# Kernel optimization log

Hardware: AMD Instinct MI355X
Metric: run time of the kernel (lower is better)

## Reference

```python
import jax, jax.numpy as jnp
import numpy as np

# Static config (matches init_kwargs: dim=64, ffn=2.66, kernel=3, smk=3, heads=2)
DIM = 64
NUM_HEADS = 2
KS = 3
SMK = 3
POOL = 7           # ContMix pools context to 7x7 -> 49 context tokens
HIDDEN = 172       # round_up(int(64*2.66), 4)
HIDDEN2 = 2 * HIDDEN
CTX_DW = HIDDEN2 // 4   # 86
CTX_DW12 = HIDDEN // 4  # 43
NK = SMK * SMK + KS * KS  # 18


def conv1x1(x, w):
    # x: [B,C,H,W], w: [O,C] -> [B,O,H,W]
    return jnp.einsum('bchw,oc->bohw', x, w)


def extract_patches(x, k):
    # x: [B,C,H,W] -> [B,C,k*k,H,W], zero ('same') padding, stride 1
    p = k // 2
    B, C, H, W = x.shape
    xp = jnp.pad(x, ((0, 0), (0, 0), (p, p), (p, p)))
    pats = [xp[:, :, i:i + H, j:j + W] for i in range(k) for j in range(k)]
    return jnp.stack(pats, axis=2)


def dyn_dw(x, attn, k, heads):
    # Dynamic depthwise mixing: per-pixel, per-head k*k kernel shared across
    # channels within a head. x: [B,C,H,W], attn: [B,g,HW,k*k]
    B, C, H, W = x.shape
    hd = C // heads
    pat = extract_patches(x, k).reshape(B, heads, hd, k * k, H * W)
    out = jnp.einsum('bgdkn,bgnk->bgdn', pat, attn)
    return out.reshape(B, C, H, W)


def contmix(x, ctx, wq, wk, wp, wpb, wo):
    # Content-aware dynamic depthwise-mixing (ContMix, OverLoCK-style).
    B, C, H, W = x.shape
    hd_qk = (C // 2) // NUM_HEADS
    scale = hd_qk ** -0.5
    # query from x, key from 7x7-pooled context
    q = conv1x1(x, wq) * scale                     # [B, C//2, H, W]
    ph, pw = H // POOL, W // POOL
    ctx_p = ctx.reshape(B, -1, POOL, ph, POOL, pw).mean(axis=(3, 5))  # [B,ctx,7,7]
    key = conv1x1(ctx_p, wk)                       # [B, C//2, 7, 7]
    q = q.reshape(B, NUM_HEADS, hd_qk, H * W)
    key = key.reshape(B, NUM_HEADS, hd_qk, POOL * POOL)
    w = jnp.einsum('bgcn,bgcl->bgnl', q, key)      # [B,g,HW,49]
    # project 49 context scores -> smk^2 + k^2 dynamic kernel taps (1x1 conv w/ bias)
    w = jnp.einsum('bgnl,ol->bgno', w, wp) + wpb   # [B,g,HW,18]
    a1 = jax.nn.softmax(w[..., :SMK * SMK], axis=-1)
    a2 = jax.nn.softmax(w[..., SMK * SMK:], axis=-1)
    # first channel half mixed with small kernel, second half with large kernel
    x1, x2 = jnp.split(x, 2, axis=1)
    y = jnp.concatenate([dyn_dw(x1, a1, SMK, NUM_HEADS),
                         dyn_dw(x2, a2, KS, NUM_HEADS)], axis=1)
    return conv1x1(y, wo)


def setup_inputs() -> dict:
    key = jax.random.key(0)
    ks = jax.random.split(key, 32)
    def w(i, o, c):
        return jax.random.normal(ks[i], (o, c), dtype=jnp.float32) / np.sqrt(c)
    inp = {
        'x': jax.random.normal(ks[0], (2, DIM, 112, 112), dtype=jnp.float32),
        'pin_w': w(1, HIDDEN2, DIM),
        'ctx_w': w(2, CTX_DW, HIDDEN2),
        'ctx1_w': w(3, CTX_DW12, HIDDEN),
        'ctx2_w': w(4, CTX_DW12, HIDDEN),
        'pout_w': w(5, DIM, HIDDEN),
        # ContMix on hidden_x2 (dim=344, ctx=86)
        'cm0_q': w(6, HIDDEN2 // 2, HIDDEN2),
        'cm0_k': w(7, HIDDEN2 // 2, CTX_DW),
        'cm0_p': w(8, NK, POOL * POOL),
        'cm0_pb': jnp.zeros((NK,), dtype=jnp.float32),
        'cm0_o': w(9, HIDDEN2, HIDDEN2),
        # ContMix on hidden (dim=172, ctx=43) -- branch 1
        'cm1_q': w(10, HIDDEN // 2, HIDDEN),
        'cm1_k': w(11, HIDDEN // 2, CTX_DW12),
        'cm1_p': w(12, NK, POOL * POOL),
        'cm1_pb': jnp.zeros((NK,), dtype=jnp.float32),
        'cm1_o': w(13, HIDDEN, HIDDEN),
        # ContMix on hidden -- branch 2
        'cm2_q': w(14, HIDDEN // 2, HIDDEN),
        'cm2_k': w(15, HIDDEN // 2, CTX_DW12),
        'cm2_p': w(16, NK, POOL * POOL),
        'cm2_pb': jnp.zeros((NK,), dtype=jnp.float32),
        'cm2_o': w(17, HIDDEN, HIDDEN),
    }
    return inp


def reference(x, pin_w, ctx_w, ctx1_w, ctx2_w, pout_w,
              cm0_q, cm0_k, cm0_p, cm0_pb, cm0_o,
              cm1_q, cm1_k, cm1_p, cm1_pb, cm1_o,
              cm2_q, cm2_k, cm2_p, cm2_pb, cm2_o):
    x_in = conv1x1(x, pin_w)                           # [B, 2*hidden, H, W]
    ctx_dw = conv1x1(x_in, ctx_w)                      # [B, ctx_dw, H, W]
    x_dw = contmix(x_in, ctx_dw, cm0_q, cm0_k, cm0_p, cm0_pb, cm0_o)
    x1, x2 = jnp.split(x_dw, 2, axis=1)                # each [B, hidden, H, W]
    ctx1 = conv1x1(x1, ctx1_w)
    ctx2 = conv1x1(x2, ctx2_w)
    x1p = jnp.tanh(contmix(x1, ctx1, cm1_q, cm1_k, cm1_p, cm1_pb, cm1_o)) + x1
    x2p = jnp.tanh(contmix(x2, ctx2, cm2_q, cm2_k, cm2_p, cm2_pb, cm2_o)) + x2
    out = conv1x1(x1p * x2p, pout_w)                   # [B, dim, H, W]
    return out
```

## Files before the change

### kernel.cpp

```cpp
#include <hip/hip_runtime.h>
#include <math.h>

#define HW 12544
#define W_IMG 112
#define B_SZ 2

typedef __attribute__((ext_vector_type(8))) short s8v;
typedef __attribute__((ext_vector_type(4))) float f4v;

__device__ __forceinline__ void split_bf16(float x, unsigned short& h, unsigned short& l) {
    unsigned u  = __float_as_uint(x);
    unsigned hb = (u + 0x7FFFu + ((u >> 16) & 1u)) >> 16;
    float hf    = __uint_as_float(hb << 16);
    float r     = x - hf;
    unsigned ur = __float_as_uint(r);
    unsigned lb = (ur + 0x7FFFu + ((ur >> 16) & 1u)) >> 16;
    h = (unsigned short)hb; l = (unsigned short)lb;
}

struct WSplitArgs {
    const float* src[8];
    const float* src2[8];
    unsigned short* hi[8];
    unsigned short* lo[8];
    int O1[8]; int O2[8]; int O2B[8]; int K[8]; int Kp[8]; int MpKp[8];
    float scale2[8];
};

__global__ __launch_bounds__(256) void wsplit_k(WSplitArgs a) {
    const int ci  = blockIdx.y;
    const int idx = blockIdx.x * 256 + threadIdx.x;
    if (idx >= a.MpKp[ci]) return;
    const int Kp   = a.Kp[ci];
    const int blk  = 32 * Kp;
    const int mblk = idx / blk;
    const int rem  = idx - mblk * blk;
    const int kc   = rem >> 10;
    const int rem2 = rem & 1023;
    const int kq   = rem2 >> 8;
    const int row  = (rem2 >> 3) & 31;
    const int j    = rem2 & 7;
    const int o = mblk * 32 + row, k = kc * 32 + kq * 8 + j;
    float v = 0.f;
    if (k < a.K[ci]) {
        if (o < a.O1[ci])
            v = a.src[ci][(size_t)o * a.K[ci] + k];
        else if (o >= a.O2B[ci] && o - a.O2B[ci] < a.O2[ci])
            v = a.src2[ci][(size_t)(o - a.O2B[ci]) * a.K[ci] + k] * a.scale2[ci];
    }
    unsigned short h, l;
    split_bf16(v, h, l);
    a.hi[ci][idx] = h; a.lo[ci][idx] = l;
}

__global__ __launch_bounds__(256) void tsplit_k(
    const float* __restrict__ src, size_t bstride, int C, int KC,
    unsigned short* __restrict__ hi, unsigned short* __restrict__ lo)
{
    __shared__ __align__(16) float t[32][36];
    const int b   = blockIdx.z;
    const int hw0 = blockIdx.x * 32;
    const int kc  = blockIdx.y;
    const int c0  = kc * 32;
    const int tid = threadIdx.x;

    {
        const int cl = tid >> 3, hq = (tid & 7) * 4;
        const int c  = c0 + cl;
        float4 v = make_float4(0.f, 0.f, 0.f, 0.f);
        if (c < C)
            v = *(const float4*)(src + (size_t)b * bstride + (size_t)c * HW + hw0 + hq);
        *(float4*)&t[cl][hq] = v;
    }
    __syncthreads();

    const int hl = tid >> 3, cq = (tid & 7) * 4;
    float v0 = t[cq + 0][hl], v1 = t[cq + 1][hl], v2 = t[cq + 2][hl], v3 = t[cq + 3][hl];
    ushort4 h4, l4;
    split_bf16(v0, h4.x, l4.x);
    split_bf16(v1, h4.y, l4.y);
    split_bf16(v2, h4.z, l4.z);
    split_bf16(v3, h4.w, l4.w);
    const int ns = hw0 >> 8, r = (hw0 & 255) + hl;
    const int kq = cq >> 3, j0 = cq & 7;
    const size_t base = (((size_t)b * 49 + ns) * KC + kc) * 8192
                        + (size_t)kq * 2048 + (size_t)r * 8 + j0;
    *(ushort4*)(hi + base) = h4;
    *(ushort4*)(lo + base) = l4;
}

template <int KP>
__global__ __launch_bounds__(256) void gemm_k(
    const unsigned short* __restrict__ bt_hi, const unsigned short* __restrict__ bt_lo,
    const unsigned short* __restrict__ w_hi,  const unsigned short* __restrict__ w_lo,
    int per_m,
    float* __restrict__ outA, int OA, size_t oa_bstride,
    float* __restrict__ outB, int OB, size_t ob_bstride, int obase,
    int mode, int Ovalid,
    const float* __restrict__ res, size_t res_bstride,
    const float* __restrict__ mul, size_t mul_bstride)
{
    constexpr int KC = KP / 32;
    __shared__ __align__(16) unsigned short Bh_s[8192];
    __shared__ __align__(16) unsigned short Bl_s[8192];
    __shared__ __align__(16) unsigned short Ah_s[1024];
    __shared__ __align__(16) unsigned short Al_s[1024];

    const int b   = blockIdx.y;
    const int bx  = blockIdx.x;
    const int xcd = bx & 7, t = bx >> 3;
    const int m   = t % per_m;
    const int ns  = (t / per_m) * 8 + xcd;
    if (ns >= 49) return;

    const int tid  = threadIdx.x;
    const int wv   = tid >> 6, lane = tid & 63;
    const int m16  = lane & 15, quad = lane >> 4;
    const int mbase = m * 32;
    const int nbase = ns * 256 + wv * 64;

    const unsigned short* Bh_g = bt_hi + ((size_t)b * 49 + ns) * KC * 8192;
    const unsigned short* Bl_g = bt_lo + ((size_t)b * 49 + ns) * KC * 8192;
    const unsigned short* Ah_g = w_hi + (size_t)m * KC * 1024;
    const unsigned short* Al_g = w_lo + (size_t)m * KC * 1024;

    f4v acc[2][4];
#pragma unroll
    for (int mt = 0; mt < 2; ++mt)
#pragma unroll
        for (int f = 0; f < 4; ++f) acc[mt][f] = (f4v){0.f, 0.f, 0.f, 0.f};

    s8v rB[8], rA;
#pragma unroll
    for (int j = 0; j < 4; ++j) {
        rB[j]     = *(const s8v*)(Bh_g + (size_t)(j * 256 + tid) * 8);
        rB[4 + j] = *(const s8v*)(Bl_g + (size_t)(j * 256 + tid) * 8);
    }
    rA = (tid < 128) ? *(const s8v*)(Ah_g + (size_t)tid * 8)
                     : *(const s8v*)(Al_g + (size_t)(tid - 128) * 8);
#pragma unroll
    for (int j = 0; j < 4; ++j) {
        *(s8v*)(Bh_s + (j * 256 + tid) * 8) = rB[j];
        *(s8v*)(Bl_s + (j * 256 + tid) * 8) = rB[4 + j];
    }
    if (tid < 128) *(s8v*)(Ah_s + tid * 8) = rA;
    else           *(s8v*)(Al_s + (tid - 128) * 8) = rA;
    __syncthreads();

#pragma unroll
    for (int kc = 0; kc < KC; ++kc) {
        if (kc + 1 < KC) {
            const unsigned short* bh = Bh_g + (size_t)(kc + 1) * 8192;
            const unsigned short* bl = Bl_g + (size_t)(kc + 1) * 8192;
#pragma unroll
            for (int j = 0; j < 4; ++j) {
                rB[j]     = *(const s8v*)(bh + (size_t)(j * 256 + tid) * 8);
                rB[4 + j] = *(const s8v*)(bl + (size_t)(j * 256 + tid) * 8);
            }
            rA = (tid < 128)
                ? *(const s8v*)(Ah_g + (size_t)(kc + 1) * 1024 + (size_t)tid * 8)
                : *(const s8v*)(Al_g + (size_t)(kc + 1) * 1024 + (size_t)(tid - 128) * 8);
        }
#pragma unroll
        for (int mt = 0; mt < 2; ++mt) {
            s8v ah = *(const s8v*)(Ah_s + (quad * 32 + mt * 16 + m16) * 8);
            s8v al = *(const s8v*)(Al_s + (quad * 32 + mt * 16 + m16) * 8);
#pragma unroll
            for (int f = 0; f < 4; ++f) {
                const int row = wv * 64 + f * 16 + m16;
                s8v bh = *(const s8v*)(Bh_s + (quad * 256 + row) * 8);
                s8v bl = *(const s8v*)(Bl_s + (quad * 256 + row) * 8);
                acc[mt][f] = __builtin_amdgcn_mfma_f32_16x16x32_bf16(ah, bh, acc[mt][f], 0, 0, 0);
                acc[mt][f] = __builtin_amdgcn_mfma_f32_16x16x32_bf16(al, bh, acc[mt][f], 0, 0, 0);
                acc[mt][f] = __builtin_amdgcn_mfma_f32_16x16x32_bf16(ah, bl, acc[mt][f], 0, 0, 0);
            }
        }
        __syncthreads();
        if (kc + 1 < KC) {
#pragma unroll
            for (int j = 0; j < 4; ++j) {
                *(s8v*)(Bh_s + (j * 256 + tid) * 8) = rB[j];
                *(s8v*)(Bl_s + (j * 256 + tid) * 8) = rB[4 + j];
            }
            if (tid < 128) *(s8v*)(Ah_s + tid * 8) = rA;
            else           *(s8v*)(Al_s + (tid - 128) * 8) = rA;
            __syncthreads();
        }
    }

#pragma unroll
    for (int mt = 0; mt < 2; ++mt) {
#pragma unroll
        for (int f = 0; f < 4; ++f) {
            const int n = nbase + f * 16 + m16;
#pragma unroll
            for (int r = 0; r < 4; ++r) {
                const int o = mbase + mt * 16 + quad * 4 + r;
                float v = acc[mt][f][r];
                if (mode == 2) {
                    if (o < Ovalid)
                        v = tanhf(v) + res[(size_t)b * res_bstride + (size_t)o * HW + n];
                } else if (mode == 3) {
                    if (o < Ovalid)
                        v = (tanhf(v) + res[(size_t)b * res_bstride + (size_t)o * HW + n])
                            * mul[(size_t)b * mul_bstride + (size_t)o * HW + n];
                }
                if (o < OA) {
                    outA[(size_t)b * oa_bstride + (size_t)o * HW + n] = v;
                } else if (o >= obase && o - obase < OB) {
                    outB[(size_t)b * ob_bstride + (size_t)(o - obase) * HW + n] = v;
                }
            }
        }
    }
}

__global__ __launch_bounds__(256) void dyndw_bt_k(
    const float* __restrict__ x, const float* __restrict__ attn,
    unsigned short* __restrict__ hi, unsigned short* __restrict__ lo,
    int C, int C_half, int hd, size_t x_bstride, int KC)
{
    const int b  = blockIdx.z, ns = blockIdx.x, tid = threadIdx.x;
    const int c0 = blockIdx.y * 8;
    const int hw = ns * 256 + tid;
    const int h = hw / W_IMG, w = hw - h * W_IMG;

    int off[9]; bool val[9];
#pragma unroll
    for (int i = 0; i < 3; ++i)
#pragma unroll
        for (int j = 0; j < 3; ++j) {
            const int hh = h + i - 1, ww = w + j - 1;
            val[i * 3 + j] = (hh >= 0 && hh < 112 && ww >= 0 && ww < 112);
            off[i * 3 + j] = hh * W_IMG + ww;
        }

    s8v hvv, lvv;
#pragma unroll
    for (int u = 0; u < 8; ++u) {
        const int c = c0 + u;
        float acc = 0.f;
        if (c < C) {
            const int half = c / C_half;
            const int g = (c - half * C_half) / hd;
            const float* ap = attn + ((size_t)(b * 2 + g) * 18 + half * 9) * HW + hw;
            const float* xp = x + (size_t)b * x_bstride + (size_t)c * HW;
#pragma unroll
            for (int k = 0; k < 9; ++k) {
                const float xv = val[k] ? xp[off[k]] : 0.f;
                acc += ap[(size_t)k * HW] * xv;
            }
        }
        unsigned short hs, ls;
        split_bf16(acc, hs, ls);
        hvv[u] = (short)hs; lvv[u] = (short)ls;
    }

    const int kc = c0 >> 5, kq = (c0 & 31) >> 3;
    const size_t base = (((size_t)b * 49 + ns) * KC + kc) * 8192
                        + (size_t)kq * 2048 + (size_t)tid * 8;
    *(s8v*)(hi + base) = hvv;
    *(s8v*)(lo + base) = lvv;
}

__global__ __launch_bounds__(64) void pool_k(
    const float* __restrict__ ctx, float* __restrict__ pooled, int C)
{
    const int c = blockIdx.x, b = blockIdx.y, t = threadIdx.x;
    if (t >= 49) return;
    const int ph = t / 7, pw = t % 7;
    const float* src = ctx + ((size_t)b * C + c) * HW;
    float sum = 0.f;
    for (int i = 0; i < 16; ++i) {
        const float* row = src + (ph * 16 + i) * W_IMG + pw * 16;
        for (int j = 0; j < 16; ++j) sum += row[j];
    }
    pooled[((size_t)b * C + c) * 49 + t] = sum * (1.0f / 256.0f);
}

__global__ __launch_bounds__(64) void keygemm_k(
    const float* __restrict__ pooled, const float* __restrict__ wk,
    float* __restrict__ key, int K, int O)
{
    const int o = blockIdx.x, b = blockIdx.y, l = threadIdx.x;
    if (l >= 49) return;
    float s = 0.f;
    for (int c = 0; c < K; ++c)
        s += wk[(size_t)o * K + c] * pooled[((size_t)b * K + c) * 49 + l];
    key[((size_t)b * O + o) * 49 + l] = s;
}

__global__ __launch_bounds__(256) void attn_k(
    const float* __restrict__ q, const float* __restrict__ key,
    const float* __restrict__ wp, const float* __restrict__ pb,
    float* __restrict__ attn, int hd)
{
    __shared__ float klds[86 * 52];
    __shared__ float plds[18 * 52];
    __shared__ float pblds[18];

    const int b = blockIdx.z, g = blockIdx.y, tid = threadIdx.x;

    for (int idx = tid; idx < hd * 49; idx += 256) {
        int c = idx / 49, l = idx - c * 49;
        klds[c * 52 + l] = key[((size_t)(b * 2 + g) * hd + c) * 49 + l];
    }
    for (int idx = tid; idx < hd * 3; idx += 256) {
        int c = idx / 3;
        klds[c * 52 + 49 + (idx - c * 3)] = 0.f;
    }
    for (int idx = tid; idx < 18 * 49; idx += 256) {
        int o = idx / 49, l = idx - o * 49;
        plds[o * 52 + l] = wp[o * 49 + l];
    }
    for (int idx = tid; idx < 18 * 3; idx += 256) {
        int o = idx / 3;
        plds[o * 52 + 49 + (idx - o * 3)] = 0.f;
    }
    if (tid < 18) pblds[tid] = pb[tid];
    __syncthreads();

    const int hw = blockIdx.x * 256 + tid;

    float4 s[13];
#pragma unroll
    for (int t = 0; t < 13; ++t) s[t] = make_float4(0.f, 0.f, 0.f, 0.f);

    const float* qp = q + (size_t)(b * 2 + g) * hd * HW + hw;
    for (int c = 0; c < hd; ++c) {
        float qv = qp[(size_t)c * HW];
        const float4* kr = (const float4*)(klds + c * 52);
#pragma unroll
        for (int t = 0; t < 13; ++t) {
            float4 kv = kr[t];
            s[t].x += qv * kv.x; s[t].y += qv * kv.y;
            s[t].z += qv * kv.z; s[t].w += qv * kv.w;
        }
    }

    float e[18];
#pragma unroll
    for (int o = 0; o < 18; ++o) {
        const float4* pr = (const float4*)(plds + o * 52);
        float4 a = make_float4(0.f, 0.f, 0.f, 0.f);
#pragma unroll
        for (int t = 0; t < 13; ++t) {
            float4 pv = pr[t];
            a.x += s[t].x * pv.x; a.y += s[t].y * pv.y;
            a.z += s[t].z * pv.z; a.w += s[t].w * pv.w;
        }
        e[o] = pblds[o] + a.x + a.y + a.z + a.w;
    }

    float* outp = attn + (size_t)(b * 2 + g) * 18 * HW + hw;
#pragma unroll
    for (int half = 0; half < 2; ++half) {
        int base = half * 9;
        float m = e[base];
#pragma unroll
        for (int k = 1; k < 9; ++k) m = fmaxf(m, e[base + k]);
        float sum = 0.f, ex[9];
#pragma unroll
        for (int k = 0; k < 9; ++k) { ex[k] = expf(e[base + k] - m); sum += ex[k]; }
        float inv = 1.0f / sum;
#pragma unroll
        for (int k = 0; k < 9; ++k) outp[(size_t)(base + k) * HW] = ex[k] * inv;
    }
}

extern "C" void kernel_launch(void* const* d_in, const int* in_sizes, int n_in,
                              void* d_out, int out_size, void* d_ws, size_t ws_size,
                              hipStream_t stream) {
    const float* x      = (const float*)d_in[0];
    const float* pin_w  = (const float*)d_in[1];
    const float* ctx_w  = (const float*)d_in[2];
    const float* ctx1_w = (const float*)d_in[3];
    const float* ctx2_w = (const float*)d_in[4];
    const float* pout_w = (const float*)d_in[5];
    const float* cm0_q  = (const float*)d_in[6];
    const float* cm0_k  = (const float*)d_in[7];
    const float* cm0_p  = (const float*)d_in[8];
    const float* cm0_pb = (const float*)d_in[9];
    const float* cm0_o  = (const float*)d_in[10];
    const float* cm1_q  = (const float*)d_in[11];
    const float* cm1_k  = (const float*)d_in[12];
    const float* cm1_p  = (const float*)d_in[13];
    const float* cm1_pb = (const float*)d_in[14];
    const float* cm1_o  = (const float*)d_in[15];
    const float* cm2_q  = (const float*)d_in[16];
    const float* cm2_k  = (const float*)d_in[17];
    const float* cm2_p  = (const float*)d_in[18];
    const float* cm2_pb = (const float*)d_in[19];
    const float* cm2_o  = (const float*)d_in[20];
    float* out = (float*)d_out;

    float* ws = (float*)d_ws;
    float* x_in  = ws;
    float* x1p   = ws;
    float* prod  = ws + 8630272;
    float* x_dw  = ws + 17260544;
    float* ctxb  = ws + 25890816;
    float* ctx1  = ws + 28048384;
    float* ctx2  = ws + 29127168;
    float* q0    = ws + 30205952;
    float* q1    = ws + 30205952;
    float* q2    = ws + 32363520;
    float* attnb = ws + 34521088;
    float* pooled= ws + 35424256;
    float* keyb  = ws + 35432704;
    unsigned short* ub = (unsigned short*)(ws + 35449568);
    static const int WOFF[8] = {0, 45056, 247808, 518144, 579584, 641024, 714752, 788480};
    static const int WO1[8]  = {344, 86, 172, 43, 43, 172, 172, 64};
    static const int WO2[8]  = {0, 172, 172, 86, 86, 0, 0, 0};
    static const int O2B[8]  = {352, 86, 192, 43, 43, 192, 192, 64};
    static const int WK[8]   = {64, 344, 344, 172, 172, 172, 172, 172};
    static const int WKP[8]  = {64, 352, 352, 192, 192, 192, 192, 192};
    static const int WMP[8]  = {352, 288, 384, 160, 160, 192, 192, 64};
    unsigned short* xt_hi   = ub + 813056;
    unsigned short* xt_lo   = ub + 2418688;
    unsigned short* bigA_hi = ub + 4024320;
    unsigned short* bigA_lo = ub + 12855296;
    unsigned short* x1t_hi  = ub + 21686272;
    unsigned short* x1t_lo  = ub + 26503168;
    unsigned short* x2t_hi  = ub + 31320064;
    unsigned short* x2t_lo  = ub + 36136960;

    const float sc0 = 1.0f / sqrtf(86.0f);
    const float sc1 = 1.0f / sqrtf(43.0f);
    const size_t BS344 = (size_t)344 * HW, BS172 = (size_t)172 * HW,
                 BS86 = (size_t)86 * HW, BS64 = (size_t)64 * HW, BS43 = (size_t)43 * HW;

    WSplitArgs wa;
    const float* wsrc1[8] = {pin_w, ctx_w, cm0_o, ctx1_w, ctx2_w, cm1_o, cm2_o, pout_w};
    const float* wsrc2[8] = {nullptr, cm0_q, cm0_o + (size_t)172 * 344, cm1_q, cm2_q,
                             nullptr, nullptr, nullptr};
    const float wsc2[8]   = {1.f, sc0, 1.f, sc1, sc1, 1.f, 1.f, 1.f};
    for (int i = 0; i < 8; ++i) {
        wa.src[i] = wsrc1[i]; wa.src2[i] = wsrc2[i];
        wa.hi[i]  = ub + WOFF[i];
        wa.lo[i]  = ub + WOFF[i] + WMP[i] * WKP[i];
        wa.O1[i] = WO1[i]; wa.O2[i] = WO2[i]; wa.O2B[i] = O2B[i];
        wa.K[i] = WK[i]; wa.Kp[i] = WKP[i];
        wa.MpKp[i] = WMP[i] * WKP[i];
        wa.scale2[i] = wsc2[i];
    }
    wsplit_k<<<dim3(528, 8), 256, 0, stream>>>(wa);

#define WHI(CI) (ub + WOFF[CI])
#define WLO(CI) (ub + WOFF[CI] + WMP[CI] * WKP[CI])
#define GRID(CI) dim3((WMP[CI] / 32) * 56, B_SZ)

    tsplit_k<<<dim3(392, 2, B_SZ), 256, 0, stream>>>(x, BS64, 64, 2, xt_hi, xt_lo);
    gemm_k<64><<<GRID(0), 256, 0, stream>>>(
        xt_hi, xt_lo, WHI(0), WLO(0), WMP[0] / 32,
        x_in, 344, BS344, nullptr, 0, 0, 352, 0, 344,
        nullptr, 0, nullptr, 0);
    tsplit_k<<<dim3(392, 11, B_SZ), 256, 0, stream>>>(x_in, BS344, 344, 11, bigA_hi, bigA_lo);

    gemm_k<352><<<GRID(1), 256, 0, stream>>>(
        bigA_hi, bigA_lo, WHI(1), WLO(1), WMP[1] / 32,
        ctxb, 86, BS86, q0, 172, BS172, 86, 0, 258,
        nullptr, 0, nullptr, 0);
    pool_k<<<dim3(86, B_SZ), dim3(64), 0, stream>>>(ctxb, pooled, 86);
    keygemm_k<<<dim3(172, B_SZ), dim3(64), 0, stream>>>(pooled, cm0_k, keyb, 86, 172);
    attn_k<<<dim3(49, 2, B_SZ), dim3(256), 0, stream>>>(q0, keyb, cm0_p, cm0_pb, attnb, 86);
    dyndw_bt_k<<<dim3(49, 44, B_SZ), 256, 0, stream>>>(
        x_in, attnb, bigA_hi, bigA_lo, 344, 172, 86, BS344, 11);
    gemm_k<352><<<GRID(2), 256, 0, stream>>>(
        bigA_hi, bigA_lo, WHI(2), WLO(2), WMP[2] / 32,
        x_dw, 172, BS344, x_dw + BS172, 172, BS344, 192, 0, 384,
        nullptr, 0, nullptr, 0);

    tsplit_k<<<dim3(392, 6, B_SZ), 256, 0, stream>>>(x_dw, BS344, 172, 6, x1t_hi, x1t_lo);
    tsplit_k<<<dim3(392, 6, B_SZ), 256, 0, stream>>>(x_dw + BS172, BS344, 172, 6, x2t_hi, x2t_lo);

    gemm_k<192><<<GRID(3), 256, 0, stream>>>(
        x1t_hi, x1t_lo, WHI(3), WLO(3), WMP[3] / 32,
        ctx1, 43, BS43, q1, 86, BS86, 43, 0, 129,
        nullptr, 0, nullptr, 0);
    pool_k<<<dim3(43, B_SZ), dim3(64), 0, stream>>>(ctx1, pooled, 43);
    keygemm_k<<<dim3(86, B_SZ), dim3(64), 0, stream>>>(pooled, cm1_k, keyb, 43, 86);
    attn_k<<<dim3(49, 2, B_SZ), dim3(256), 0, stream>>>(q1, keyb, cm1_p, cm1_pb, attnb, 43);
    dyndw_bt_k<<<dim3(49, 24, B_SZ), 256, 0, stream>>>(
        x_dw, attnb, x1t_hi, x1t_lo, 172, 86, 43, BS344, 6);
    gemm_k<192><<<GRID(5), 256, 0, stream>>>(
        x1t_hi, x1t_lo, WHI(5), WLO(5), WMP[5] / 32,
        x1p, 172, BS172, nullptr, 0, 0, 192, 2, 172,
        x_dw, BS344, nullptr, 0);

    gemm_k<192><<<GRID(4), 256, 0, stream>>>(
        x2t_hi, x2t_lo, WHI(4), WLO(4), WMP[4] / 32,
        ctx2, 43, BS43, q2, 86, BS86, 43, 0, 129,
        nullptr, 0, nullptr, 0);
    pool_k<<<dim3(43, B_SZ), dim3(64), 0, stream>>>(ctx2, pooled, 43);
    keygemm_k<<<dim3(86, B_SZ), dim3(64), 0, stream>>>(pooled, cm2_k, keyb, 43, 86);
    attn_k<<<dim3(49, 2, B_SZ), dim3(256), 0, stream>>>(q2, keyb, cm2_p, cm2_pb, attnb, 43);
    dyndw_bt_k<<<dim3(49, 24, B_SZ), 256, 0, stream>>>(
        x_dw + BS172, attnb, x2t_hi, x2t_lo, 172, 86, 43, BS344, 6);
    gemm_k<192><<<GRID(6), 256, 0, stream>>>(
        x2t_hi, x2t_lo, WHI(6), WLO(6), WMP[6] / 32,
        prod, 172, BS172, nullptr, 0, 0, 192, 3, 172,
        x_dw + BS172, BS344, x1p, BS172);

    tsplit_k<<<dim3(392, 6, B_SZ), 256, 0, stream>>>(prod, BS172, 172, 6, bigA_hi, bigA_lo);
    gemm_k<192><<<GRID(7), 256, 0, stream>>>(
        bigA_hi, bigA_lo, WHI(7), WLO(7), WMP[7] / 32,
        out, 64, BS64, nullptr, 0, 0, 64, 0, 64,
        nullptr, 0, nullptr, 0);

#undef WHI
#undef WLO
#undef GRID
}
```

Baseline: 532.1 us.

## Batch the two independent ContMix branches into single dual-branch kernel launches

```diff
diff --git a/kernel.cpp b/kernel.cpp
--- a/kernel.cpp
+++ b/kernel.cpp
@@ -89,16 +89,93 @@
     *(ushort4*)(lo + base) = l4;
 }
 
+__global__ __launch_bounds__(256) void tsplit2_k(
+    const float* __restrict__ src, size_t bstride,
+    unsigned short* __restrict__ hi_a, unsigned short* __restrict__ lo_a,
+    unsigned short* __restrict__ hi_b, unsigned short* __restrict__ lo_b)
+{
+    __shared__ __align__(16) float t[32][36];
+    const int zz = blockIdx.z, b = zz & 1, br = zz >> 1;
+    const int hw0 = blockIdx.x * 32;
+    const int kc  = blockIdx.y;
+    const int c0  = kc * 32;
+    const int tid = threadIdx.x;
+
+    {
+        const int cl = tid >> 3, hq = (tid & 7) * 4;
+        const int c  = c0 + cl;
+        float4 v = make_float4(0.f, 0.f, 0.f, 0.f);
+        if (c < 172)
+            v = *(const float4*)(src + (size_t)b * bstride
+                                 + (size_t)(br * 172 + c) * HW + hw0 + hq);
+        *(float4*)&t[cl][hq] = v;
+    }
+    __syncthreads();
+
+    const int hl = tid >> 3, cq = (tid & 7) * 4;
+    float v0 = t[cq + 0][hl], v1 = t[cq + 1][hl], v2 = t[cq + 2][hl], v3 = t[cq + 3][hl];
+    ushort4 h4, l4;
+    split_bf16(v0, h4.x, l4.x);
+    split_bf16(v1, h4.y, l4.y);
+    split_bf16(v2, h4.z, l4.z);
+    split_bf16(v3, h4.w, l4.w);
+    const int ns = hw0 >> 8, r = (hw0 & 255) + hl;
+    const int kq = cq >> 3, j0 = cq & 7;
+    const size_t base = (((size_t)b * 49 + ns) * 6 + kc) * 8192
+                        + (size_t)kq * 2048 + (size_t)r * 8 + j0;
+    unsigned short* hi = br ? hi_b : hi_a;
+    unsigned short* lo = br ? lo_b : lo_a;
+    *(ushort4*)(hi + base) = h4;
+    *(ushort4*)(lo + base) = l4;
+}
+
+__global__ __launch_bounds__(256) void mulsplit_k(
+    const float* __restrict__ t1, const float* __restrict__ t2, size_t bstride,
+    unsigned short* __restrict__ hi, unsigned short* __restrict__ lo)
+{
+    __shared__ __align__(16) float t[32][36];
+    const int b   = blockIdx.z;
+    const int hw0 = blockIdx.x * 32;
+    const int kc  = blockIdx.y;
+    const int c0  = kc * 32;
+    const int tid = threadIdx.x;
+
+    {
+        const int cl = tid >> 3, hq = (tid & 7) * 4;
+        const int c  = c0 + cl;
+        float4 v = make_float4(0.f, 0.f, 0.f, 0.f);
+        if (c < 172) {
+            const size_t off = (size_t)b * bstride + (size_t)c * HW + hw0 + hq;
+            float4 a = *(const float4*)(t1 + off);
+            float4 m = *(const float4*)(t2 + off);
+            v = make_float4(a.x * m.x, a.y * m.y, a.z * m.z, a.w * m.w);
+        }
+        *(float4*)&t[cl][hq] = v;
+    }
+    __syncthreads();
+
+    const int hl = tid >> 3, cq = (tid & 7) * 4;
+    float v0 = t[cq + 0][hl], v1 = t[cq + 1][hl], v2 = t[cq + 2][hl], v3 = t[cq + 3][hl];
+    ushort4 h4, l4;
+    split_bf16(v0, h4.x, l4.x);
+    split_bf16(v1, h4.y, l4.y);
+    split_bf16(v2, h4.z, l4.z);
+    split_bf16(v3, h4.w, l4.w);
+    const int ns = hw0 >> 8, r = (hw0 & 255) + hl;
+    const int kq = cq >> 3, j0 = cq & 7;
+    const size_t base = (((size_t)b * 49 + ns) * 6 + kc) * 8192
+                        + (size_t)kq * 2048 + (size_t)r * 8 + j0;
+    *(ushort4*)(hi + base) = h4;
+    *(ushort4*)(lo + base) = l4;
+}
+
 template <int KP>
 __global__ __launch_bounds__(256) void gemm_k(
     const unsigned short* __restrict__ bt_hi, const unsigned short* __restrict__ bt_lo,
     const unsigned short* __restrict__ w_hi,  const unsigned short* __restrict__ w_lo,
     int per_m,
     float* __restrict__ outA, int OA, size_t oa_bstride,
-    float* __restrict__ outB, int OB, size_t ob_bstride, int obase,
-    int mode, int Ovalid,
-    const float* __restrict__ res, size_t res_bstride,
-    const float* __restrict__ mul, size_t mul_bstride)
+    float* __restrict__ outB, int OB, size_t ob_bstride, int obase)
 {
     constexpr int KC = KP / 32;
     __shared__ __align__(16) unsigned short Bh_s[8192];
@@ -197,14 +274,135 @@
             for (int r = 0; r < 4; ++r) {
                 const int o = mbase + mt * 16 + quad * 4 + r;
                 float v = acc[mt][f][r];
-                if (mode == 2) {
-                    if (o < Ovalid)
-                        v = tanhf(v) + res[(size_t)b * res_bstride + (size_t)o * HW + n];
-                } else if (mode == 3) {
-                    if (o < Ovalid)
-                        v = (tanhf(v) + res[(size_t)b * res_bstride + (size_t)o * HW + n])
-                            * mul[(size_t)b * mul_bstride + (size_t)o * HW + n];
+                if (o < OA) {
+                    outA[(size_t)b * oa_bstride + (size_t)o * HW + n] = v;
+                } else if (o >= obase && o - obase < OB) {
+                    outB[(size_t)b * ob_bstride + (size_t)(o - obase) * HW + n] = v;
                 }
+            }
+        }
+    }
+}
+
+template <int KP>
+__global__ __launch_bounds__(256) void gemm2_k(
+    const unsigned short* __restrict__ bth_a, const unsigned short* __restrict__ btl_a,
+    const unsigned short* __restrict__ wh_a,  const unsigned short* __restrict__ wl_a,
+    const unsigned short* __restrict__ bth_b, const unsigned short* __restrict__ btl_b,
+    const unsigned short* __restrict__ wh_b,  const unsigned short* __restrict__ wl_b,
+    int per_m,
+    float* __restrict__ outA_a, float* __restrict__ outA_b, int OA, size_t oa_bstride,
+    float* __restrict__ outB_a, float* __restrict__ outB_b, int OB, size_t ob_bstride, int obase,
+    int mode, int Ovalid,
+    const float* __restrict__ res_a, const float* __restrict__ res_b, size_t res_bstride)
+{
+    constexpr int KC = KP / 32;
+    __shared__ __align__(16) unsigned short Bh_s[8192];
+    __shared__ __align__(16) unsigned short Bl_s[8192];
+    __shared__ __align__(16) unsigned short Ah_s[1024];
+    __shared__ __align__(16) unsigned short Al_s[1024];
+
+    const int zz  = blockIdx.y, b = zz & 1, br = zz >> 1;
+    const int bx  = blockIdx.x;
+    const int xcd = bx & 7, t = bx >> 3;
+    const int m   = t % per_m;
+    const int ns  = (t / per_m) * 8 + xcd;
+    if (ns >= 49) return;
+
+    const unsigned short* bt_hi = br ? bth_b : bth_a;
+    const unsigned short* bt_lo = br ? btl_b : btl_a;
+    const unsigned short* w_hi  = br ? wh_b : wh_a;
+    const unsigned short* w_lo  = br ? wl_b : wl_a;
+    float* outA = br ? outA_b : outA_a;
+    float* outB = br ? outB_b : outB_a;
+    const float* res = br ? res_b : res_a;
+
+    const int tid  = threadIdx.x;
+    const int wv   = tid >> 6, lane = tid & 63;
+    const int m16  = lane & 15, quad = lane >> 4;
+    const int mbase = m * 32;
+    const int nbase = ns * 256 + wv * 64;
+
+    const unsigned short* Bh_g = bt_hi + ((size_t)b * 49 + ns) * KC * 8192;
+    const unsigned short* Bl_g = bt_lo + ((size_t)b * 49 + ns) * KC * 8192;
+    const unsigned short* Ah_g = w_hi + (size_t)m * KC * 1024;
+    const unsigned short* Al_g = w_lo + (size_t)m * KC * 1024;
+
+    f4v acc[2][4];
+#pragma unroll
+    for (int mt = 0; mt < 2; ++mt)
+#pragma unroll
+        for (int f = 0; f < 4; ++f) acc[mt][f] = (f4v){0.f, 0.f, 0.f, 0.f};
+
+    s8v rB[8], rA;
+#pragma unroll
+    for (int j = 0; j < 4; ++j) {
+        rB[j]     = *(const s8v*)(Bh_g + (size_t)(j * 256 + tid) * 8);
+        rB[4 + j] = *(const s8v*)(Bl_g + (size_t)(j * 256 + tid) * 8);
+    }
+    rA = (tid < 128) ? *(const s8v*)(Ah_g + (size_t)tid * 8)
+                     : *(const s8v*)(Al_g + (size_t)(tid - 128) * 8);
+#pragma unroll
+    for (int j = 0; j < 4; ++j) {
+        *(s8v*)(Bh_s + (j * 256 + tid) * 8) = rB[j];
+        *(s8v*)(Bl_s + (j * 256 + tid) * 8) = rB[4 + j];
+    }
+    if (tid < 128) *(s8v*)(Ah_s + tid * 8) = rA;
+    else           *(s8v*)(Al_s + (tid - 128) * 8) = rA;
+    __syncthreads();
+
+#pragma unroll
+    for (int kc = 0; kc < KC; ++kc) {
+        if (kc + 1 < KC) {
+            const unsigned short* bh = Bh_g + (size_t)(kc + 1) * 8192;
+            const unsigned short* bl = Bl_g + (size_t)(kc + 1) * 8192;
+#pragma unroll
+            for (int j = 0; j < 4; ++j) {
+                rB[j]     = *(const s8v*)(bh + (size_t)(j * 256 + tid) * 8);
+                rB[4 + j] = *(const s8v*)(bl + (size_t)(j * 256 + tid) * 8);
+            }
+            rA = (tid < 128)
+                ? *(const s8v*)(Ah_g + (size_t)(kc + 1) * 1024 + (size_t)tid * 8)
+                : *(const s8v*)(Al_g + (size_t)(kc + 1) * 1024 + (size_t)(tid - 128) * 8);
+        }
+#pragma unroll
+        for (int mt = 0; mt < 2; ++mt) {
+            s8v ah = *(const s8v*)(Ah_s + (quad * 32 + mt * 16 + m16) * 8);
+            s8v al = *(const s8v*)(Al_s + (quad * 32 + mt * 16 + m16) * 8);
+#pragma unroll
+            for (int f = 0; f < 4; ++f) {
+                const int row = wv * 64 + f * 16 + m16;
+                s8v bh = *(const s8v*)(Bh_s + (quad * 256 + row) * 8);
+                s8v bl = *(const s8v*)(Bl_s + (quad * 256 + row) * 8);
+                acc[mt][f] = __builtin_amdgcn_mfma_f32_16x16x32_bf16(ah, bh, acc[mt][f], 0, 0, 0);
+                acc[mt][f] = __builtin_amdgcn_mfma_f32_16x16x32_bf16(al, bh, acc[mt][f], 0, 0, 0);
+                acc[mt][f] = __builtin_amdgcn_mfma_f32_16x16x32_bf16(ah, bl, acc[mt][f], 0, 0, 0);
+            }
+        }
+        __syncthreads();
+        if (kc + 1 < KC) {
+#pragma unroll
+            for (int j = 0; j < 4; ++j) {
+                *(s8v*)(Bh_s + (j * 256 + tid) * 8) = rB[j];
+                *(s8v*)(Bl_s + (j * 256 + tid) * 8) = rB[4 + j];
+            }
+            if (tid < 128) *(s8v*)(Ah_s + tid * 8) = rA;
+            else           *(s8v*)(Al_s + (tid - 128) * 8) = rA;
+            __syncthreads();
+        }
+    }
+
+#pragma unroll
+    for (int mt = 0; mt < 2; ++mt) {
+#pragma unroll
+        for (int f = 0; f < 4; ++f) {
+            const int n = nbase + f * 16 + m16;
+#pragma unroll
+            for (int r = 0; r < 4; ++r) {
+                const int o = mbase + mt * 16 + quad * 4 + r;
+                float v = acc[mt][f][r];
+                if (mode == 2 && o < Ovalid)
+                    v = tanhf(v) + res[(size_t)b * res_bstride + (size_t)o * HW + n];
                 if (o < OA) {
                     outA[(size_t)b * oa_bstride + (size_t)o * HW + n] = v;
                 } else if (o >= obase && o - obase < OB) {
@@ -263,6 +461,60 @@
     *(s8v*)(lo + base) = lvv;
 }
 
+__global__ __launch_bounds__(256) void dyndw2_bt_k(
+    const float* __restrict__ x, size_t x_bstride,
+    const float* __restrict__ attn_a, const float* __restrict__ attn_b,
+    unsigned short* __restrict__ hi_a, unsigned short* __restrict__ lo_a,
+    unsigned short* __restrict__ hi_b, unsigned short* __restrict__ lo_b)
+{
+    const int zz = blockIdx.z, b = zz & 1, br = zz >> 1;
+    const int ns = blockIdx.x, tid = threadIdx.x;
+    const int c0 = blockIdx.y * 8;
+    const int hw = ns * 256 + tid;
+    const int h = hw / W_IMG, w = hw - h * W_IMG;
+
+    const float* attn = br ? attn_b : attn_a;
+    unsigned short* hi = br ? hi_b : hi_a;
+    unsigned short* lo = br ? lo_b : lo_a;
+
+    int off[9]; bool val[9];
+#pragma unroll
+    for (int i = 0; i < 3; ++i)
+#pragma unroll
+        for (int j = 0; j < 3; ++j) {
+            const int hh = h + i - 1, ww = w + j - 1;
+            val[i * 3 + j] = (hh >= 0 && hh < 112 && ww >= 0 && ww < 112);
+            off[i * 3 + j] = hh * W_IMG + ww;
+        }
+
+    s8v hvv, lvv;
+#pragma unroll
+    for (int u = 0; u < 8; ++u) {
+        const int c = c0 + u;
+        float acc = 0.f;
+        if (c < 172) {
+            const int half = c / 86;
+            const int g = (c - half * 86) / 43;
+            const float* ap = attn + ((size_t)(b * 2 + g) * 18 + half * 9) * HW + hw;
+            const float* xp = x + (size_t)b * x_bstride + (size_t)(br * 172 + c) * HW;
+#pragma unroll
+            for (int k = 0; k < 9; ++k) {
+                const float xv = val[k] ? xp[off[k]] : 0.f;
+                acc += ap[(size_t)k * HW] * xv;
+            }
+        }
+        unsigned short hs, ls;
+        split_bf16(acc, hs, ls);
+        hvv[u] = (short)hs; lvv[u] = (short)ls;
+    }
+
+    const int kc = c0 >> 5, kq = (c0 & 31) >> 3;
+    const size_t base = (((size_t)b * 49 + ns) * 6 + kc) * 8192
+                        + (size_t)kq * 2048 + (size_t)tid * 8;
+    *(s8v*)(hi + base) = hvv;
+    *(s8v*)(lo + base) = lvv;
+}
+
 __global__ __launch_bounds__(64) void pool_k(
     const float* __restrict__ ctx, float* __restrict__ pooled, int C)
 {
@@ -278,6 +530,25 @@
     pooled[((size_t)b * C + c) * 49 + t] = sum * (1.0f / 256.0f);
 }
 
+__global__ __launch_bounds__(64) void pool2_k(
+    const float* __restrict__ ctx_a, const float* __restrict__ ctx_b,
+    float* __restrict__ p_a, float* __restrict__ p_b, int C)
+{
+    const int zz = blockIdx.y, b = zz & 1, br = zz >> 1;
+    const int c = blockIdx.x, t = threadIdx.x;
+    if (t >= 49) return;
+    const float* ctx = br ? ctx_b : ctx_a;
+    float* pooled    = br ? p_b : p_a;
+    const int ph = t / 7, pw = t % 7;
+    const float* src = ctx + ((size_t)b * C + c) * HW;
+    float sum = 0.f;
+    for (int i = 0; i < 16; ++i) {
+        const float* row = src + (ph * 16 + i) * W_IMG + pw * 16;
+        for (int j = 0; j < 16; ++j) sum += row[j];
+    }
+    pooled[((size_t)b * C + c) * 49 + t] = sum * (1.0f / 256.0f);
+}
+
 __global__ __launch_bounds__(64) void keygemm_k(
     const float* __restrict__ pooled, const float* __restrict__ wk,
     float* __restrict__ key, int K, int O)
@@ -290,82 +561,118 @@
     key[((size_t)b * O + o) * 49 + l] = s;
 }
 
+__global__ __launch_bounds__(64) void keygemm2_k(
+    const float* __restrict__ p_a, const float* __restrict__ p_b,
+    const float* __restrict__ wk_a, const float* __restrict__ wk_b,
+    float* __restrict__ k_a, float* __restrict__ k_b, int K, int O)
+{
+    const int zz = blockIdx.y, b = zz & 1, br = zz >> 1;
+    const int o = blockIdx.x, l = threadIdx.x;
+    if (l >= 49) return;
+    const float* pooled = br ? p_b : p_a;
+    const float* wk     = br ? wk_b : wk_a;
+    float* key          = br ? k_b : k_a;
+    float s = 0.f;
+    for (int c = 0; c < K; ++c)
+        s += wk[(size_t)o * K + c] * pooled[((size_t)b * K + c) * 49 + l];
+    key[((size_t)b * O + o) * 49 + l] = s;
+}
+
+__device__ __forceinline__ void attn_body(
+    const float* __restrict__ q, const float* __restrict__ key,
+    const float* __restrict__ wp, const float* __restrict__ pb,
+    float* __restrict__ attn, int hd, int b, int g, int tid, int nsx)
+{
+    __shared__ float klds[86 * 52];
+    __shared__ float plds[18 * 52];
+    __shared__ float pblds[18];
+
+    for (int idx = tid; idx < hd * 49; idx += 256) {
+        int c = idx / 49, l = idx - c * 49;
+        klds[c * 52 + l] = key[((size_t)(b * 2 + g) * hd + c) * 49 + l];
+    }
+    for (int idx = tid; idx < hd * 3; idx += 256) {
+        int c = idx / 3;
+        klds[c * 52 + 49 + (idx - c * 3)] = 0.f;
+    }
+    for (int idx = tid; idx < 18 * 49; idx += 256) {
+        int o = idx / 49, l = idx - o * 49;
+        plds[o * 52 + l] = wp[o * 49 + l];
+    }
+    for (int idx = tid; idx < 18 * 3; idx += 256) {
+        int o = idx / 3;
+        plds[o * 52 + 49 + (idx - o * 3)] = 0.f;
+    }
+    if (tid < 18) pblds[tid] = pb[tid];
+    __syncthreads();
+
+    const int hw = nsx * 256 + tid;
+
+    float4 s[13];
+#pragma unroll
+    for (int t = 0; t < 13; ++t) s[t] = make_float4(0.f, 0.f, 0.f, 0.f);
+
+    const float* qp = q + (size_t)(b * 2 + g) * hd * HW + hw;
+    for (int c = 0; c < hd; ++c) {
+        float qv = qp[(size_t)c * HW];
+        const float4* kr = (const float4*)(klds + c * 52);
+#pragma unroll
+        for (int t = 0; t < 13; ++t) {
+            float4 kv = kr[t];
+            s[t].x += qv * kv.x; s[t].y += qv * kv.y;
+            s[t].z += qv * kv.z; s[t].w += qv * kv.w;
+        }
+    }
+
+    float e[18];
+#pragma unroll
+    for (int o = 0; o < 18; ++o) {
+        const float4* pr = (const float4*)(plds + o * 52);
+        float4 a = make_float4(0.f, 0.f, 0.f, 0.f);
+#pragma unroll
+        for (int t = 0; t < 13; ++t) {
+            float4 pv = pr[t];
+            a.x += s[t].x * pv.x; a.y += s[t].y * pv.y;
+            a.z += s[t].z * pv.z; a.w += s[t].w * pv.w;
+        }
+        e[o] = pblds[o] + a.x + a.y + a.z + a.w;
+    }
+
+    float* outp = attn + (size_t)(b * 2 + g) * 18 * HW + hw;
+#pragma unroll
+    for (int half = 0; half < 2; ++half) {
+        int base = half * 9;
+        float m = e[base];
+#pragma unroll
+        for (int k = 1; k < 9; ++k) m = fmaxf(m, e[base + k]);
+        float sum = 0.f, ex[9];
+#pragma unroll
+        for (int k = 0; k < 9; ++k) { ex[k] = expf(e[base + k] - m); sum += ex[k]; }
+        float inv = 1.0f / sum;
+#pragma unroll
+        for (int k = 0; k < 9; ++k) outp[(size_t)(base + k) * HW] = ex[k] * inv;
+    }
+}
+
 __global__ __launch_bounds__(256) void attn_k(
     const float* __restrict__ q, const float* __restrict__ key,
     const float* __restrict__ wp, const float* __restrict__ pb,
     float* __restrict__ attn, int hd)
 {
-    __shared__ float klds[86 * 52];
-    __shared__ float plds[18 * 52];
-    __shared__ float pblds[18];
-
-    const int b = blockIdx.z, g = blockIdx.y, tid = threadIdx.x;
-
-    for (int idx = tid; idx < hd * 49; idx += 256) {
-        int c = idx / 49, l = idx - c * 49;
-        klds[c * 52 + l] = key[((size_t)(b * 2 + g) * hd + c) * 49 + l];
-    }
-    for (int idx = tid; idx < hd * 3; idx += 256) {
-        int c = idx / 3;
-        klds[c * 52 + 49 + (idx - c * 3)] = 0.f;
-    }
-    for (int idx = tid; idx < 18 * 49; idx += 256) {
-        int o = idx / 49, l = idx - o * 49;
-        plds[o * 52 + l] = wp[o * 49 + l];
-    }
-    for (int idx = tid; idx < 18 * 3; idx += 256) {
-        int o = idx / 3;
-        plds[o * 52 + 49 + (idx - o * 3)] = 0.f;
-    }
-    if (tid < 18) pblds[tid] = pb[tid];
-    __syncthreads();
-
-    const int hw = blockIdx.x * 256 + tid;
-
-    float4 s[13];
-#pragma unroll
-    for (int t = 0; t < 13; ++t) s[t] = make_float4(0.f, 0.f, 0.f, 0.f);
-
-    const float* qp = q + (size_t)(b * 2 + g) * hd * HW + hw;
-    for (int c = 0; c < hd; ++c) {
-        float qv = qp[(size_t)c * HW];
-        const float4* kr = (const float4*)(klds + c * 52);
-#pragma unroll
-        for (int t = 0; t < 13; ++t) {
-            float4 kv = kr[t];
-            s[t].x += qv * kv.x; s[t].y += qv * kv.y;
-            s[t].z += qv * kv.z; s[t].w += qv * kv.w;
-        }
-    }
-
-    float e[18];
-#pragma unroll
-    for (int o = 0; o < 18; ++o) {
-        const float4* pr = (const float4*)(plds + o * 52);
-        float4 a = make_float4(0.f, 0.f, 0.f, 0.f);
-#pragma unroll
-        for (int t = 0; t < 13; ++t) {
-            float4 pv = pr[t];
-            a.x += s[t].x * pv.x; a.y += s[t].y * pv.y;
-            a.z += s[t].z * pv.z; a.w += s[t].w * pv.w;
-        }
-        e[o] = pblds[o] + a.x + a.y + a.z + a.w;
-    }
-
-    float* outp = attn + (size_t)(b * 2 + g) * 18 * HW + hw;
-#pragma unroll
-    for (int half = 0; half < 2; ++half) {
-        int base = half * 9;
-        float m = e[base];
-#pragma unroll
-        for (int k = 1; k < 9; ++k) m = fmaxf(m, e[base + k]);
-        float sum = 0.f, ex[9];
-#pragma unroll
-        for (int k = 0; k < 9; ++k) { ex[k] = expf(e[base + k] - m); sum += ex[k]; }
-        float inv = 1.0f / sum;
-#pragma unroll
-        for (int k = 0; k < 9; ++k) outp[(size_t)(base + k) * HW] = ex[k] * inv;
-    }
+    attn_body(q, key, wp, pb, attn, hd, blockIdx.z, blockIdx.y, threadIdx.x, blockIdx.x);
+}
+
+__global__ __launch_bounds__(256) void attn2_k(
+    const float* __restrict__ q_a, const float* __restrict__ q_b,
+    const float* __restrict__ k_a, const float* __restrict__ k_b,
+    const float* __restrict__ wp_a, const float* __restrict__ wp_b,
+    const float* __restrict__ pb_a, const float* __restrict__ pb_b,
+    float* __restrict__ at_a, float* __restrict__ at_b, int hd)
+{
+    const int zz = blockIdx.z, b = zz & 1, br = zz >> 1;
+    attn_body(br ? q_b : q_a, br ? k_b : k_a, br ? wp_b : wp_a,
+              br ? pb_b : pb_a, br ? at_b : at_a, hd, b, blockIdx.y,
+              threadIdx.x, blockIdx.x);
 }
 
 extern "C" void kernel_launch(void* const* d_in, const int* in_sizes, int n_in,
@@ -396,8 +703,8 @@
 
     float* ws = (float*)d_ws;
     float* x_in  = ws;
-    float* x1p   = ws;
-    float* prod  = ws + 8630272;
+    float* t1    = ws;
+    float* t2    = ws + 8630272;
     float* x_dw  = ws + 17260544;
     float* ctxb  = ws + 25890816;
     float* ctx1  = ws + 28048384;
@@ -405,10 +712,16 @@
     float* q0    = ws + 30205952;
     float* q1    = ws + 30205952;
     float* q2    = ws + 32363520;
-    float* attnb = ws + 34521088;
-    float* pooled= ws + 35424256;
-    float* keyb  = ws + 35432704;
-    unsigned short* ub = (unsigned short*)(ws + 35449568);
+    float* attn0 = ws + 34521088;
+    float* attn1 = ws + 35424256;
+    float* attn2 = ws + 36327424;
+    float* pool0 = ws + 37230592;
+    float* pool1 = ws + 37239020;
+    float* pool2b= ws + 37243234;
+    float* key0  = ws + 37247448;
+    float* key1  = ws + 37264304;
+    float* key2  = ws + 37272732;
+    unsigned short* ub = (unsigned short*)(ws + 37281160);
     static const int WOFF[8] = {0, 45056, 247808, 518144, 579584, 641024, 714752, 788480};
     static const int WO1[8]  = {344, 86, 172, 43, 43, 172, 172, 64};
     static const int WO2[8]  = {0, 172, 172, 86, 86, 0, 0, 0};
@@ -449,66 +762,57 @@
 #define WHI(CI) (ub + WOFF[CI])
 #define WLO(CI) (ub + WOFF[CI] + WMP[CI] * WKP[CI])
 #define GRID(CI) dim3((WMP[CI] / 32) * 56, B_SZ)
+#define GRID2(CI) dim3((WMP[CI] / 32) * 56, 2 * B_SZ)
 
     tsplit_k<<<dim3(392, 2, B_SZ), 256, 0, stream>>>(x, BS64, 64, 2, xt_hi, xt_lo);
     gemm_k<64><<<GRID(0), 256, 0, stream>>>(
         xt_hi, xt_lo, WHI(0), WLO(0), WMP[0] / 32,
-        x_in, 344, BS344, nullptr, 0, 0, 352, 0, 344,
-        nullptr, 0, nullptr, 0);
+        x_in, 344, BS344, nullptr, 0, 0, 352);
     tsplit_k<<<dim3(392, 11, B_SZ), 256, 0, stream>>>(x_in, BS344, 344, 11, bigA_hi, bigA_lo);
 
     gemm_k<352><<<GRID(1), 256, 0, stream>>>(
         bigA_hi, bigA_lo, WHI(1), WLO(1), WMP[1] / 32,
-        ctxb, 86, BS86, q0, 172, BS172, 86, 0, 258,
-        nullptr, 0, nullptr, 0);
-    pool_k<<<dim3(86, B_SZ), dim3(64), 0, stream>>>(ctxb, pooled, 86);
-    keygemm_k<<<dim3(172, B_SZ), dim3(64), 0, stream>>>(pooled, cm0_k, keyb, 86, 172);
-    attn_k<<<dim3(49, 2, B_SZ), dim3(256), 0, stream>>>(q0, keyb, cm0_p, cm0_pb, attnb, 86);
+        ctxb, 86, BS86, q0, 172, BS172, 86);
+    pool_k<<<dim3(86, B_SZ), dim3(64), 0, stream>>>(ctxb, pool0, 86);
+    keygemm_k<<<dim3(172, B_SZ), dim3(64), 0, stream>>>(pool0, cm0_k, key0, 86, 172);
+    attn_k<<<dim3(49, 2, B_SZ), dim3(256), 0, stream>>>(q0, key0, cm0_p, cm0_pb, attn0, 86);
     dyndw_bt_k<<<dim3(49, 44, B_SZ), 256, 0, stream>>>(
-        x_in, attnb, bigA_hi, bigA_lo, 344, 172, 86, BS344, 11);
+        x_in, attn0, bigA_hi, bigA_lo, 344, 172, 86, BS344, 11);
     gemm_k<352><<<GRID(2), 256, 0, stream>>>(
         bigA_hi, bigA_lo, WHI(2), WLO(2), WMP[2] / 32,
-        x_dw, 172, BS344, x_dw + BS172, 172, BS344, 192, 0, 384,
-        nullptr, 0, nullptr, 0);
-
-    tsplit_k<<<dim3(392, 6, B_SZ), 256, 0, stream>>>(x_dw, BS344, 172, 6, x1t_hi, x1t_lo);
-    tsplit_k<<<dim3(392, 6, B_SZ), 256, 0, stream>>>(x_dw + BS172, BS344, 172, 6, x2t_hi, x2t_lo);
-
-    gemm_k<192><<<GRID(3), 256, 0, stream>>>(
-        x1t_hi, x1t_lo, WHI(3), WLO(3), WMP[3] / 32,
-        ctx1, 43, BS43, q1, 86, BS86, 43, 0, 129,
-        nullptr, 0, nullptr, 0);
-    pool_k<<<dim3(43, B_SZ), dim3(64), 0, stream>>>(ctx1, pooled, 43);
-    keygemm_k<<<dim3(86, B_SZ), dim3(64), 0, stream>>>(pooled, cm1_k, keyb, 43, 86);
-    attn_k<<<dim3(49, 2, B_SZ), dim3(256), 0, stream>>>(q1, keyb, cm1_p, cm1_pb, attnb, 43);
-    dyndw_bt_k<<<dim3(49, 24, B_SZ), 256, 0, stream>>>(
-        x_dw, attnb, x1t_hi, x1t_lo, 172, 86, 43, BS344, 6);
-    gemm_k<192><<<GRID(5), 256, 0, stream>>>(
-        x1t_hi, x1t_lo, WHI(5), WLO(5), WMP[5] / 32,
-        x1p, 172, BS172, nullptr, 0, 0, 192, 2, 172,
-        x_dw, BS344, nullptr, 0);
-
-    gemm_k<192><<<GRID(4), 256, 0, stream>>>(
-        x2t_hi, x2t_lo, WHI(4), WLO(4), WMP[4] / 32,
-        ctx2, 43, BS43, q2, 86, BS86, 43, 0, 129,
-        nullptr, 0, nullptr, 0);
-    pool_k<<<dim3(43, B_SZ), dim3(64), 0, stream>>>(ctx2, pooled, 43);
-    keygemm_k<<<dim3(86, B_SZ), dim3(64), 0, stream>>>(pooled, cm2_k, keyb, 43, 86);
-    attn_k<<<dim3(49, 2, B_SZ), dim3(256), 0, stream>>>(q2, keyb, cm2_p, cm2_pb, attnb, 43);
-    dyndw_bt_k<<<dim3(49, 24, B_SZ), 256, 0, stream>>>(
-        x_dw + BS172, attnb, x2t_hi, x2t_lo, 172, 86, 43, BS344, 6);
-    gemm_k<192><<<GRID(6), 256, 0, stream>>>(
-        x2t_hi, x2t_lo, WHI(6), WLO(6), WMP[6] / 32,
-        prod, 172, BS172, nullptr, 0, 0, 192, 3, 172,
-        x_dw + BS172, BS344, x1p, BS172);
-
-    tsplit_k<<<dim3(392, 6, B_SZ), 256, 0, stream>>>(prod, BS172, 172, 6, bigA_hi, bigA_lo);
+        x_dw, 172, BS344, x_dw + BS172, 172, BS344, 192);
+
+    tsplit2_k<<<dim3(392, 6, 2 * B_SZ), 256, 0, stream>>>(
+        x_dw, BS344, x1t_hi, x1t_lo, x2t_hi, x2t_lo);
+
+    gemm2_k<192><<<GRID2(3), 256, 0, stream>>>(
+        x1t_hi, x1t_lo, WHI(3), WLO(3),
+        x2t_hi, x2t_lo, WHI(4), WLO(4), WMP[3] / 32,
+        ctx1, ctx2, 43, BS43,
+        q1, q2, 86, BS86, 43,
+        0, 129, nullptr, nullptr, 0);
+    pool2_k<<<dim3(43, 2 * B_SZ), dim3(64), 0, stream>>>(ctx1, ctx2, pool1, pool2b, 43);
+    keygemm2_k<<<dim3(86, 2 * B_SZ), dim3(64), 0, stream>>>(
+        pool1, pool2b, cm1_k, cm2_k, key1, key2, 43, 86);
+    attn2_k<<<dim3(49, 2, 2 * B_SZ), dim3(256), 0, stream>>>(
+        q1, q2, key1, key2, cm1_p, cm2_p, cm1_pb, cm2_pb, attn1, attn2, 43);
+    dyndw2_bt_k<<<dim3(49, 24, 2 * B_SZ), 256, 0, stream>>>(
+        x_dw, BS344, attn1, attn2, x1t_hi, x1t_lo, x2t_hi, x2t_lo);
+    gemm2_k<192><<<GRID2(5), 256, 0, stream>>>(
+        x1t_hi, x1t_lo, WHI(5), WLO(5),
+        x2t_hi, x2t_lo, WHI(6), WLO(6), WMP[5] / 32,
+        t1, t2, 172, BS172,
+        nullptr, nullptr, 0, 0, 192,
+        2, 172, x_dw, x_dw + BS172, BS344);
+
+    mulsplit_k<<<dim3(392, 6, B_SZ), 256, 0, stream>>>(t1, t2, BS172, bigA_hi, bigA_lo);
+
     gemm_k<192><<<GRID(7), 256, 0, stream>>>(
         bigA_hi, bigA_lo, WHI(7), WLO(7), WMP[7] / 32,
-        out, 64, BS64, nullptr, 0, 0, 64, 0, 64,
-        nullptr, 0, nullptr, 0);
+        out, 64, BS64, nullptr, 0, 0, 64);
 
 #undef WHI
 #undef WLO
 #undef GRID
-}
+#undef GRID2
+}
```

After: 487.2 us (median of 2 runs). -8.4%, faster.
